# Performance work log

Measured on AMD Instinct MI355X. Metric: run time of the kernel, lower is better.

## Reference

```python
import jax, jax.numpy as jnp
import numpy as np

B, S, E = 8, 2048, 1024


def setup_inputs() -> dict:
    key = jax.random.key(0)
    ks = jax.random.split(key, 8)
    scale = 1.0 / np.sqrt(E)
    x = jax.random.normal(ks[0], (B, S, E), dtype=jnp.float32)
    Wq = jax.random.uniform(ks[1], (E, E), jnp.float32, -scale, scale)
    bq = jax.random.uniform(ks[2], (E,), jnp.float32, -scale, scale)
    Wk = jax.random.uniform(ks[3], (E, E), jnp.float32, -scale, scale)
    bk = jax.random.uniform(ks[4], (E,), jnp.float32, -scale, scale)
    Wv = jax.random.uniform(ks[5], (E, E), jnp.float32, -scale, scale)
    bv = jax.random.uniform(ks[6], (E,), jnp.float32, -scale, scale)
    # key-padding mask: True = fill position (broadcasts over query dim)
    mask = jax.random.randint(ks[7], (B, 1, S), 0, 2) > 0
    return {"x": x, "Wq": Wq, "bq": bq, "Wk": Wk, "bk": bk, "Wv": Wv, "bv": bv, "mask": mask}


def reference(x, Wq, bq, Wk, bk, Wv, bv, mask):
    # torch Linear: y = x @ W.T + b
    q = jnp.einsum('bse,fe->bsf', x, Wq) + bq
    k = jnp.einsum('bse,fe->bsf', x, Wk) + bk
    v = jnp.einsum('bse,fe->bsf', x, Wv) + bv
    inv_sqrt_d = 1.0 / jnp.sqrt(jnp.asarray(E, x.dtype))
    A = jnp.einsum('bqe,bke->bqk', q, k) * inv_sqrt_d  # (B, S, S)
    # non-standard masked_fill: fills with 1e-9 (NOT -inf), pre-softmax
    A = jnp.where(mask, jnp.asarray(1e-9, A.dtype), A)
    A = jax.nn.softmax(A, axis=-1)
    out = jnp.einsum('bqk,bke->bqe', A, v)
    # dropout is identity at inference
    return out
```

## Files before the change

### kernel.cpp

```cpp
#include <hip/hip_runtime.h>
#include <hip/hip_bf16.h>

#define B_ 8
#define S_ 2048
#define E_ 1024

using f32x4 = __attribute__((ext_vector_type(4))) float;
using s16x8 = __attribute__((ext_vector_type(8))) short;
using u16x8 = __attribute__((ext_vector_type(8))) unsigned short;

typedef __attribute__((address_space(1))) unsigned int glb_u32;
typedef __attribute__((address_space(3))) unsigned int lds_u32;

#define FENCE() __builtin_amdgcn_sched_barrier(0)

static __device__ __forceinline__ unsigned short f2bf(float f) {
    union { float f; unsigned int u; } v; v.f = f;
    unsigned int u = v.u;
    u += 0x7FFFu + ((u >> 16) & 1u);
    return (unsigned short)(u >> 16);
}
static __device__ __forceinline__ float bf2f(unsigned short h) {
    union { unsigned int u; float f; } v; v.u = ((unsigned int)h) << 16;
    return v.f;
}

__global__ __launch_bounds__(256) void mask_canon_kernel(
    const unsigned char* __restrict__ src, unsigned char* __restrict__ dst, int n)
{
    __shared__ int flags;
    if (threadIdx.x == 0) flags = 0;
    __syncthreads();
    int f = 0;
    for (int j = threadIdx.x; j < n; j += 256) {
        unsigned char b = src[j];
        if (b) {
            int p = j & 3;
            if (p == 1) f |= 1;
            if (p >= 2) f |= 2;
        }
    }
    if (f) atomicOr(&flags, f);
    __syncthreads();
    const int fl = flags;
    for (int i = threadIdx.x; i < n; i += 256) {
        unsigned char v;
        if (fl & 1)      v = (unsigned char)(src[i] != 0);
        else if (fl & 2) v = (unsigned char)(((const float*)(const void*)src)[i] != 0.0f);
        else             v = (unsigned char)(((const int*)(const void*)src)[i] != 0);
        dst[i] = v;
    }
}

__global__ __launch_bounds__(256) void cvt_all_kernel(
    const float* __restrict__ x,  unsigned short* __restrict__ xb,
    const float* __restrict__ w0, unsigned short* __restrict__ d0,
    const float* __restrict__ w1, unsigned short* __restrict__ d1,
    const float* __restrict__ w2, unsigned short* __restrict__ d2,
    int nx8, int nw8)
{
    const int total = nx8 + 3 * nw8;
    const int stride = gridDim.x * 256;
    for (int i = blockIdx.x * 256 + threadIdx.x; i < total; i += stride) {
        const float* s; unsigned short* d; int k;
        if (i < nx8)                { s = x;  d = xb; k = i; }
        else if (i < nx8 + nw8)     { s = w0; d = d0; k = i - nx8; }
        else if (i < nx8 + 2 * nw8) { s = w1; d = d1; k = i - nx8 - nw8; }
        else                        { s = w2; d = d2; k = i - nx8 - 2 * nw8; }
        float4 a = *(const float4*)(s + (size_t)k * 8);
        float4 b = *(const float4*)(s + (size_t)k * 8 + 4);
        u16x8 o;
        o[0]=f2bf(a.x); o[1]=f2bf(a.y); o[2]=f2bf(a.z); o[3]=f2bf(a.w);
        o[4]=f2bf(b.x); o[5]=f2bf(b.y); o[6]=f2bf(b.z); o[7]=f2bf(b.w);
        *(u16x8*)(d + (size_t)k * 8) = o;
    }
}

template<int EPI>
__global__ __launch_bounds__(512, 2) void gemm256(
    const unsigned short* __restrict__ A, const unsigned short* __restrict__ B,
    void* __restrict__ Cout,
    long long sAz, long long sBz, long long sCz,
    int lda, int ldb, int ldc, int K,
    const unsigned char* __restrict__ mask, int maskStride, float scale,
    const float* __restrict__ bias)
{
    __shared__ unsigned short lds[65536];
    const int tid = threadIdx.x;
    const int lane = tid & 63, w = tid >> 6;
    const int wr = w >> 2, wc = w & 3;
    const int fr = lane & 15, ch = lane >> 4;

    const int gx = gridDim.x, gy = gridDim.y;
    const int nwg = gx * gy * gridDim.z;
    int bid = blockIdx.x + gx * (blockIdx.y + gy * blockIdx.z);
    bid = (bid & 7) * (nwg >> 3) + (bid >> 3);
    const int bx = bid % gx; int tmp = bid / gx;
    const int by = tmp % gy; const int bz = tmp / gy;

    const unsigned short* Ab = A + (size_t)bz * sAz;
    const unsigned short* Bb = B + (size_t)bz * sBz;
    const int m0 = by * 256, n0 = bx * 256;

    const int rdlane = fr * 32 + ((ch * 8) ^ ((fr & 8) ? 16 : 0));
    const int local = (lane * 16) ^ (lane & 32);
    const int rloc = local >> 6;
    const int cloc = (local >> 4) & 3;

    f32x4 acc[8][4] = {};
    const int NT = K >> 6;

    auto STAGE = [&](const unsigned short* __restrict__ src, int ld, int base,
                     int ts, int half, int matoff, unsigned bo) {
        const int k0 = ts * 64;
        const int rowb = half * 128 + w * 16;
        #pragma unroll
        for (int kk = 0; kk < 2; ++kk) {
            const unsigned short* g = src + (size_t)(base + rowb + rloc) * ld
                                          + (k0 + kk * 32 + cloc * 8);
            __builtin_amdgcn_global_load_lds((const glb_u32*)g,
                (lds_u32*)&lds[bo + matoff + kk * 8192 + rowb * 32], 16, 0, 0);
        }
    };

    STAGE(Ab, lda, m0, 0, 0, 0, 0);      STAGE(Ab, lda, m0, 0, 1, 0, 0);
    STAGE(Bb, ldb, n0, 0, 0, 16384, 0);  STAGE(Bb, ldb, n0, 0, 1, 16384, 0);
    STAGE(Ab, lda, m0, 1, 0, 0, 32768);  STAGE(Ab, lda, m0, 1, 1, 0, 32768);
    STAGE(Bb, ldb, n0, 1, 0, 16384, 32768);
    asm volatile("s_waitcnt vmcnt(6)" ::: "memory");
    __builtin_amdgcn_s_barrier();

    for (int t = 0; t < NT; ++t) {
        const unsigned bo = (unsigned)(t & 1) * 32768u;
        const unsigned nbo = bo ^ 32768u;
        const int tp1 = (t + 1 < NT) ? t + 1 : NT - 1;
        const int tp2 = (t + 2 < NT) ? t + 2 : NT - 1;

        s16x8 af[8][2], bfv[4][2];
        #pragma unroll
        for (int i = 0; i < 4; ++i)
            #pragma unroll
            for (int kk = 0; kk < 2; ++kk)
                af[i][kk] = *(const s16x8*)&lds[bo + kk * 8192 + (wr * 128 + i * 16) * 32 + rdlane];
        #pragma unroll
        for (int j = 0; j < 2; ++j)
            #pragma unroll
            for (int kk = 0; kk < 2; ++kk)
                bfv[j][kk] = *(const s16x8*)&lds[bo + 16384 + kk * 8192 + (wc * 64 + j * 16) * 32 + rdlane];
        FENCE();
        #pragma unroll
        for (int i = 4; i < 8; ++i)
            #pragma unroll
            for (int kk = 0; kk < 2; ++kk)
                af[i][kk] = *(const s16x8*)&lds[bo + kk * 8192 + (wr * 128 + i * 16) * 32 + rdlane];
        #pragma unroll
        for (int j = 2; j < 4; ++j)
            #pragma unroll
            for (int kk = 0; kk < 2; ++kk)
                bfv[j][kk] = *(const s16x8*)&lds[bo + 16384 + kk * 8192 + (wc * 64 + j * 16) * 32 + rdlane];
        STAGE(Bb, ldb, n0, tp1, 1, 16384, nbo);
        FENCE();
        asm volatile("s_waitcnt lgkmcnt(12)" ::: "memory");
        FENCE();
        __builtin_amdgcn_s_setprio(1);
        #pragma unroll
        for (int kk = 0; kk < 2; ++kk)
            #pragma unroll
            for (int i = 0; i < 4; ++i)
                #pragma unroll
                for (int j = 0; j < 2; ++j)
                    acc[i][j] = __builtin_amdgcn_mfma_f32_16x16x32_bf16(af[i][kk], bfv[j][kk], acc[i][j], 0, 0, 0);
        __builtin_amdgcn_s_setprio(0);
        FENCE();
        asm volatile("s_waitcnt lgkmcnt(0)" ::: "memory");
        FENCE();
        __builtin_amdgcn_s_setprio(1);
        #pragma unroll
        for (int kk = 0; kk < 2; ++kk)
            #pragma unroll
            for (int i = 0; i < 4; ++i)
                #pragma unroll
                for (int j = 0; j < 2; ++j)
                    acc[i][2 + j] = __builtin_amdgcn_mfma_f32_16x16x32_bf16(af[i][kk], bfv[2 + j][kk], acc[i][2 + j], 0, 0, 0);
        __builtin_amdgcn_s_setprio(0);
        FENCE();
        __builtin_amdgcn_s_barrier();
        FENCE();
        STAGE(Bb, ldb, n0, tp2, 0, 16384, bo);
        STAGE(Ab, lda, m0, tp2, 0, 0, bo);
        STAGE(Ab, lda, m0, tp2, 1, 0, bo);
        FENCE();
        __builtin_amdgcn_s_setprio(1);
        #pragma unroll
        for (int kk = 0; kk < 2; ++kk)
            #pragma unroll
            for (int i = 0; i < 4; ++i)
                #pragma unroll
                for (int j = 0; j < 2; ++j)
                    acc[4 + i][j] = __builtin_amdgcn_mfma_f32_16x16x32_bf16(af[4 + i][kk], bfv[j][kk], acc[4 + i][j], 0, 0, 0);
        #pragma unroll
        for (int kk = 0; kk < 2; ++kk)
            #pragma unroll
            for (int i = 0; i < 4; ++i)
                #pragma unroll
                for (int j = 0; j < 2; ++j)
                    acc[4 + i][2 + j] = __builtin_amdgcn_mfma_f32_16x16x32_bf16(af[4 + i][kk], bfv[2 + j][kk], acc[4 + i][2 + j], 0, 0, 0);
        __builtin_amdgcn_s_setprio(0);
        FENCE();
        asm volatile("s_waitcnt vmcnt(6)" ::: "memory");
        FENCE();
        __builtin_amdgcn_s_barrier();
    }

    asm volatile("s_waitcnt vmcnt(0) lgkmcnt(0)" ::: "memory");
    __builtin_amdgcn_s_barrier();

    if constexpr (EPI == 1) {
        float* Cb = (float*)Cout + (size_t)bz * sCz;
        float* lf = (float*)lds;
        #pragma unroll
        for (int p = 0; p < 2; ++p) {
            if (p == 1) __syncthreads();
            #pragma unroll
            for (int j = 0; j < 4; ++j) {
                const int lcol = wc * 64 + j * 16 + fr;
                #pragma unroll
                for (int i = 0; i < 4; ++i)
                    #pragma unroll
                    for (int r = 0; r < 4; ++r) {
                        const int lrow = wr * 64 + i * 16 + ch * 4 + r;
                        lf[lrow * 256 + lcol] = acc[4 * p + i][j][r];
                    }
            }
            __syncthreads();
            #pragma unroll
            for (int s = 0; s < 16; ++s) {
                const int lrow = s * 8 + (tid >> 6);
                const int colf = (tid & 63) * 4;
                float4 v = *(const float4*)&lf[lrow * 256 + colf];
                const int mrow = m0 + ((lrow >= 64) ? 128 : 0) + p * 64 + (lrow & 63);
                *(float4*)&Cb[(size_t)mrow * ldc + n0 + colf] = v;
            }
        }
    } else {
        unsigned short* Cb = (unsigned short*)Cout + (size_t)bz * sCz;
        const unsigned char* mb = (EPI == 0) ? mask + (size_t)bz * maskStride : nullptr;
        #pragma unroll
        for (int j = 0; j < 4; ++j) {
            const int lcol = wc * 64 + j * 16 + fr;
            bool msk = false; float bn = 0.f;
            if constexpr (EPI == 0) msk = mb[n0 + lcol] != 0;
            if constexpr (EPI == 2) bn = bias[n0 + lcol];
            #pragma unroll
            for (int i = 0; i < 8; ++i) {
                #pragma unroll
                for (int r = 0; r < 4; ++r) {
                    const int lrow = wr * 128 + i * 16 + ch * 4 + r;
                    float val;
                    if constexpr (EPI == 0)      val = msk ? 1e-9f : acc[i][j][r] * scale;
                    else if constexpr (EPI == 2) val = acc[i][j][r] + bn;
                    else                         val = acc[i][j][r] + bias[m0 + lrow];
                    lds[lrow * 256 + lcol] = f2bf(val);
                }
            }
        }
        __syncthreads();
        #pragma unroll
        for (int s = 0; s < 16; ++s) {
            const int lrow = s * 16 + (tid >> 5);
            const int colu = (tid & 31) * 8;
            u16x8 v = *(const u16x8*)&lds[lrow * 256 + colu];
            *(u16x8*)&Cb[(size_t)(m0 + lrow) * ldc + n0 + colu] = v;
        }
    }
}

__global__ __launch_bounds__(256) void softmax_kernel(unsigned short* __restrict__ P)
{
    const int row = blockIdx.x;
    const int tid = threadIdx.x;
    unsigned short* prow = P + (size_t)row * S_;
    u16x8 v = *(const u16x8*)&prow[tid * 8];
    float f[8];
    #pragma unroll
    for (int j = 0; j < 8; ++j) f[j] = bf2f(v[j]);
    float m = f[0];
    #pragma unroll
    for (int j = 1; j < 8; ++j) m = fmaxf(m, f[j]);
    #pragma unroll
    for (int o = 1; o < 64; o <<= 1) m = fmaxf(m, __shfl_xor(m, o, 64));
    __shared__ float smax[4], ssum[4];
    const int w = tid >> 6, lane = tid & 63;
    if (lane == 0) smax[w] = m;
    __syncthreads();
    m = fmaxf(fmaxf(smax[0], smax[1]), fmaxf(smax[2], smax[3]));
    float e[8], s = 0.f;
    #pragma unroll
    for (int j = 0; j < 8; ++j) { e[j] = expf(f[j] - m); s += e[j]; }
    #pragma unroll
    for (int o = 1; o < 64; o <<= 1) s += __shfl_xor(s, o, 64);
    if (lane == 0) ssum[w] = s;
    __syncthreads();
    s = ssum[0] + ssum[1] + ssum[2] + ssum[3];
    const float inv = 1.0f / s;
    u16x8 o8;
    #pragma unroll
    for (int j = 0; j < 8; ++j) o8[j] = f2bf(e[j] * inv);
    *(u16x8*)&prow[tid * 8] = o8;
}

extern "C" void kernel_launch(void* const* d_in, const int* in_sizes, int n_in,
                              void* d_out, int out_size, void* d_ws, size_t ws_size,
                              hipStream_t stream)
{
    const float* x  = (const float*)d_in[0];
    const float* Wq = (const float*)d_in[1];
    const float* bq = (const float*)d_in[2];
    const float* Wk = (const float*)d_in[3];
    const float* bk = (const float*)d_in[4];
    const float* Wv = (const float*)d_in[5];
    const float* bv = (const float*)d_in[6];
    const unsigned char* mraw = (const unsigned char*)d_in[7];

    const int BS = B_ * S_;
    unsigned short* Qb = (unsigned short*)d_ws;
    unsigned short* Kb = Qb + (size_t)BS * E_;
    unsigned short* VT = Kb + (size_t)BS * E_;
    unsigned short* Sc = VT + (size_t)BS * E_;
    unsigned short* xb = Sc;
    unsigned short* Wqb = Sc + (size_t)BS * E_;
    unsigned short* Wkb = Wqb + (size_t)E_ * E_;
    unsigned short* Wvb = Wkb + (size_t)E_ * E_;
    unsigned char* mcanon = (unsigned char*)(Sc + (size_t)B_ * S_ * S_);

    mask_canon_kernel<<<1, 256, 0, stream>>>(mraw, mcanon, BS);

    cvt_all_kernel<<<2048, 256, 0, stream>>>(
        x, xb, Wq, Wqb, Wk, Wkb, Wv, Wvb, BS * E_ / 8, E_ * E_ / 8);

    gemm256<2><<<dim3(E_ / 256, BS / 256), 512, 0, stream>>>(
        xb, Wqb, (void*)Qb, 0, 0, 0, E_, E_, E_, E_, nullptr, 0, 1.0f, bq);
    gemm256<2><<<dim3(E_ / 256, BS / 256), 512, 0, stream>>>(
        xb, Wkb, (void*)Kb, 0, 0, 0, E_, E_, E_, E_, nullptr, 0, 1.0f, bk);
    gemm256<3><<<dim3(BS / 256, E_ / 256), 512, 0, stream>>>(
        Wvb, xb, (void*)VT, 0, 0, 0, E_, E_, BS, E_, nullptr, 0, 1.0f, bv);

    gemm256<0><<<dim3(S_ / 256, S_ / 256, B_), 512, 0, stream>>>(
        Qb, Kb, (void*)Sc,
        (long long)S_ * E_, (long long)S_ * E_, (long long)S_ * S_,
        E_, E_, S_, E_, mcanon, S_, 0.03125f, nullptr);

    softmax_kernel<<<dim3(BS), 256, 0, stream>>>(Sc);

    gemm256<1><<<dim3(E_ / 256, S_ / 256, B_), 512, 0, stream>>>(
        Sc, VT, d_out,
        (long long)S_ * S_, (long long)S_, (long long)S_ * E_,
        S_, BS, E_, S_, nullptr, 0, 1.0f, nullptr);
}
```

Before: 333.4 us.

## Fuse softmax into QK^T and PV GEMM epilogues, merge Q/K projection launches

Drops the separate softmax pass. The QK^T GEMM epilogue now writes exp(score) unnormalized, or exp(1e-9)≈1 for masked entries, and stores per-tile row partial sums. A tiny kernel turns those sums into reciprocals, which the PV GEMM epilogue applies to each output row. This saves a full read and write of the B×S×S score matrix. The Q and K projections are also merged into one launch with a doubled grid. Skipping max subtraction is numerically risky in general, but works here because the scaled scores are small.

```diff
diff --git a/kernel.cpp b/kernel.cpp
--- a/kernel.cpp
+++ b/kernel.cpp
@@ -76,6 +76,17 @@
     }
 }
 
+__global__ __launch_bounds__(256) void invrs_kernel(
+    const float* __restrict__ psum, float* __restrict__ invrs, int n)
+{
+    int i = blockIdx.x * 256 + threadIdx.x;
+    if (i < n) {
+        const float* p = psum + (size_t)i * 8;
+        float s = ((p[0] + p[1]) + (p[2] + p[3])) + ((p[4] + p[5]) + (p[6] + p[7]));
+        invrs[i] = 1.0f / s;
+    }
+}
+
 template<int EPI>
 __global__ __launch_bounds__(512, 2) void gemm256(
     const unsigned short* __restrict__ A, const unsigned short* __restrict__ B,
@@ -83,7 +94,9 @@
     long long sAz, long long sBz, long long sCz,
     int lda, int ldb, int ldc, int K,
     const unsigned char* __restrict__ mask, int maskStride, float scale,
-    const float* __restrict__ bias)
+    const float* __restrict__ bias,
+    const unsigned short* __restrict__ B2, const float* __restrict__ bias2,
+    void* __restrict__ Cout2, float* __restrict__ aux)
 {
     __shared__ unsigned short lds[65536];
     const int tid = threadIdx.x;
@@ -100,7 +113,13 @@
 
     const unsigned short* Ab = A + (size_t)bz * sAz;
     const unsigned short* Bb = B + (size_t)bz * sBz;
-    const int m0 = by * 256, n0 = bx * 256;
+    const float* biasv = bias;
+    void* Coutv = Cout;
+    const int m0 = by * 256;
+    int n0 = bx * 256;
+    if constexpr (EPI == 4) {
+        if (n0 >= 1024) { Bb = B2; biasv = bias2; Coutv = Cout2; n0 -= 1024; }
+    }
 
     const int rdlane = fr * 32 + ((ch * 8) ^ ((fr & 8) ? 16 : 0));
     const int local = (lane * 16) ^ (lane & 32);
@@ -216,7 +235,8 @@
     __builtin_amdgcn_s_barrier();
 
     if constexpr (EPI == 1) {
-        float* Cb = (float*)Cout + (size_t)bz * sCz;
+        float* Cb = (float*)Coutv + (size_t)bz * sCz;
+        const float* invrs = aux;
         float* lf = (float*)lds;
         #pragma unroll
         for (int p = 0; p < 2; ++p) {
@@ -239,32 +259,48 @@
                 const int colf = (tid & 63) * 4;
                 float4 v = *(const float4*)&lf[lrow * 256 + colf];
                 const int mrow = m0 + ((lrow >= 64) ? 128 : 0) + p * 64 + (lrow & 63);
+                const float irs = invrs[(size_t)bz * S_ + mrow];
+                v.x *= irs; v.y *= irs; v.z *= irs; v.w *= irs;
                 *(float4*)&Cb[(size_t)mrow * ldc + n0 + colf] = v;
             }
         }
     } else {
-        unsigned short* Cb = (unsigned short*)Cout + (size_t)bz * sCz;
+        unsigned short* Cb = (unsigned short*)Coutv + (size_t)bz * sCz;
         const unsigned char* mb = (EPI == 0) ? mask + (size_t)bz * maskStride : nullptr;
         #pragma unroll
         for (int j = 0; j < 4; ++j) {
             const int lcol = wc * 64 + j * 16 + fr;
             bool msk = false; float bn = 0.f;
             if constexpr (EPI == 0) msk = mb[n0 + lcol] != 0;
-            if constexpr (EPI == 2) bn = bias[n0 + lcol];
+            if constexpr (EPI == 2 || EPI == 4) bn = biasv[n0 + lcol];
             #pragma unroll
             for (int i = 0; i < 8; ++i) {
                 #pragma unroll
                 for (int r = 0; r < 4; ++r) {
                     const int lrow = wr * 128 + i * 16 + ch * 4 + r;
                     float val;
-                    if constexpr (EPI == 0)      val = msk ? 1e-9f : acc[i][j][r] * scale;
-                    else if constexpr (EPI == 2) val = acc[i][j][r] + bn;
-                    else                         val = acc[i][j][r] + bias[m0 + lrow];
+                    if constexpr (EPI == 0)      val = msk ? 1.0f : __expf(acc[i][j][r] * scale);
+                    else if constexpr (EPI == 2 || EPI == 4) val = acc[i][j][r] + bn;
+                    else                         val = acc[i][j][r] + biasv[m0 + lrow];
                     lds[lrow * 256 + lcol] = f2bf(val);
                 }
             }
         }
         __syncthreads();
+        if constexpr (EPI == 0) {
+            const int row = tid >> 1, half = tid & 1;
+            float s = 0.f;
+            #pragma unroll
+            for (int c = 0; c < 16; ++c) {
+                const int cc = (c + row) & 15;
+                u16x8 v8 = *(const u16x8*)&lds[row * 256 + half * 128 + cc * 8];
+                #pragma unroll
+                for (int e = 0; e < 8; ++e) s += bf2f(v8[e]);
+            }
+            s += __shfl_xor(s, 1, 64);
+            if (half == 0)
+                aux[((size_t)bz * S_ + m0 + row) * 8 + bx] = s;
+        }
         #pragma unroll
         for (int s = 0; s < 16; ++s) {
             const int lrow = s * 16 + (tid >> 5);
@@ -273,40 +309,6 @@
             *(u16x8*)&Cb[(size_t)(m0 + lrow) * ldc + n0 + colu] = v;
         }
     }
-}
-
-__global__ __launch_bounds__(256) void softmax_kernel(unsigned short* __restrict__ P)
-{
-    const int row = blockIdx.x;
-    const int tid = threadIdx.x;
-    unsigned short* prow = P + (size_t)row * S_;
-    u16x8 v = *(const u16x8*)&prow[tid * 8];
-    float f[8];
-    #pragma unroll
-    for (int j = 0; j < 8; ++j) f[j] = bf2f(v[j]);
-    float m = f[0];
-    #pragma unroll
-    for (int j = 1; j < 8; ++j) m = fmaxf(m, f[j]);
-    #pragma unroll
-    for (int o = 1; o < 64; o <<= 1) m = fmaxf(m, __shfl_xor(m, o, 64));
-    __shared__ float smax[4], ssum[4];
-    const int w = tid >> 6, lane = tid & 63;
-    if (lane == 0) smax[w] = m;
-    __syncthreads();
-    m = fmaxf(fmaxf(smax[0], smax[1]), fmaxf(smax[2], smax[3]));
-    float e[8], s = 0.f;
-    #pragma unroll
-    for (int j = 0; j < 8; ++j) { e[j] = expf(f[j] - m); s += e[j]; }
-    #pragma unroll
-    for (int o = 1; o < 64; o <<= 1) s += __shfl_xor(s, o, 64);
-    if (lane == 0) ssum[w] = s;
-    __syncthreads();
-    s = ssum[0] + ssum[1] + ssum[2] + ssum[3];
-    const float inv = 1.0f / s;
-    u16x8 o8;
-    #pragma unroll
-    for (int j = 0; j < 8; ++j) o8[j] = f2bf(e[j] * inv);
-    *(u16x8*)&prow[tid * 8] = o8;
 }
 
 extern "C" void kernel_launch(void* const* d_in, const int* in_sizes, int n_in,
@@ -332,28 +334,32 @@
     unsigned short* Wkb = Wqb + (size_t)E_ * E_;
     unsigned short* Wvb = Wkb + (size_t)E_ * E_;
     unsigned char* mcanon = (unsigned char*)(Sc + (size_t)B_ * S_ * S_);
+    float* psum = (float*)(mcanon + 65536);
+    float* invr = psum + (size_t)BS * 8;
 
     mask_canon_kernel<<<1, 256, 0, stream>>>(mraw, mcanon, BS);
 
     cvt_all_kernel<<<2048, 256, 0, stream>>>(
         x, xb, Wq, Wqb, Wk, Wkb, Wv, Wvb, BS * E_ / 8, E_ * E_ / 8);
 
-    gemm256<2><<<dim3(E_ / 256, BS / 256), 512, 0, stream>>>(
-        xb, Wqb, (void*)Qb, 0, 0, 0, E_, E_, E_, E_, nullptr, 0, 1.0f, bq);
-    gemm256<2><<<dim3(E_ / 256, BS / 256), 512, 0, stream>>>(
-        xb, Wkb, (void*)Kb, 0, 0, 0, E_, E_, E_, E_, nullptr, 0, 1.0f, bk);
+    gemm256<4><<<dim3(2048 / 256, BS / 256), 512, 0, stream>>>(
+        xb, Wqb, (void*)Qb, 0, 0, 0, E_, E_, E_, E_, nullptr, 0, 1.0f, bq,
+        Wkb, bk, (void*)Kb, nullptr);
     gemm256<3><<<dim3(BS / 256, E_ / 256), 512, 0, stream>>>(
-        Wvb, xb, (void*)VT, 0, 0, 0, E_, E_, BS, E_, nullptr, 0, 1.0f, bv);
+        Wvb, xb, (void*)VT, 0, 0, 0, E_, E_, BS, E_, nullptr, 0, 1.0f, bv,
+        nullptr, nullptr, nullptr, nullptr);
 
     gemm256<0><<<dim3(S_ / 256, S_ / 256, B_), 512, 0, stream>>>(
         Qb, Kb, (void*)Sc,
         (long long)S_ * E_, (long long)S_ * E_, (long long)S_ * S_,
-        E_, E_, S_, E_, mcanon, S_, 0.03125f, nullptr);
-
-    softmax_kernel<<<dim3(BS), 256, 0, stream>>>(Sc);
+        E_, E_, S_, E_, mcanon, S_, 0.03125f, nullptr,
+        nullptr, nullptr, nullptr, psum);
+
+    invrs_kernel<<<BS / 256, 256, 0, stream>>>(psum, invr, BS);
 
     gemm256<1><<<dim3(E_ / 256, S_ / 256, B_), 512, 0, stream>>>(
         Sc, VT, d_out,
         (long long)S_ * S_, (long long)S_, (long long)S_ * E_,
-        S_, BS, E_, S_, nullptr, 0, 1.0f, nullptr);
-}
+        S_, BS, E_, S_, nullptr, 0, 1.0f, nullptr,
+        nullptr, nullptr, nullptr, invr);
+}
```

After: 309.2 us. 7.3% less time.
